# Optimization experiments

Hardware: AMD Instinct MI355X
Metric: run time of the kernel (lower is better)

Reference implementation:

```python
import jax, jax.numpy as jnp
import numpy as np

D_MODEL = 1024
N_HEAD = 16
B, T = 4, 2048


def setup_inputs() -> dict:
    key = jax.random.key(0)
    k1, k2, k3, k4, k5 = jax.random.split(key, 5)
    s = 0.02
    return {
        "x": jax.random.normal(k1, (B, T, D_MODEL), dtype=jnp.float32),
        "w_attn": jax.random.normal(k2, (3 * D_MODEL, D_MODEL), dtype=jnp.float32) * s,
        "b_attn": jax.random.normal(k3, (3 * D_MODEL,), dtype=jnp.float32) * s,
        "w_proj": jax.random.normal(k4, (D_MODEL, D_MODEL), dtype=jnp.float32) * s,
        "b_proj": jax.random.normal(k5, (D_MODEL,), dtype=jnp.float32) * s,
    }


def reference(x, w_attn, b_attn, w_proj, b_proj):
    # x: [B, T, C]
    Bb, Tt, C = x.shape
    H = N_HEAD
    dk = C // H
    scale = 1.0 / np.sqrt(dk).astype(np.float32)

    qkv = x @ w_attn.T + b_attn                      # [B, T, 3C]
    q, k, v = jnp.split(qkv, 3, axis=-1)             # each [B, T, C]
    # -> [B, H, T, dk]
    q = q.reshape(Bb, Tt, H, dk).transpose(0, 2, 1, 3)
    k = k.reshape(Bb, Tt, H, dk).transpose(0, 2, 1, 3)
    v = v.reshape(Bb, Tt, H, dk).transpose(0, 2, 1, 3)

    att = jnp.einsum("bhqd,bhkd->bhqk", q, k) * scale   # [B, H, T, T]
    att = jax.nn.softmax(att, axis=-1)
    y = jnp.einsum("bhqk,bhkd->bhqd", att, v)            # [B, H, T, dk]
    y = y.transpose(0, 2, 1, 3).reshape(Bb, Tt, C)       # [B, T, C]
    return y @ w_proj.T + b_proj
```

## Files before the change

kernel.cpp:

```cpp
#include <hip/hip_runtime.h>
#include <hip/hip_bf16.h>

typedef __attribute__((ext_vector_type(8))) short short8;
typedef __attribute__((ext_vector_type(4))) short short4v;
typedef __attribute__((ext_vector_type(4))) float floatx4;
typedef __attribute__((ext_vector_type(16))) float floatx16;

#define B_ 4
#define T_ 2048
#define C_ 1024
#define H_ 16
#define DK_ 64
#define M_ (B_ * T_)
#define N3_ (3 * C_)

#define QSCALE 0.1803368801111243f

__device__ __forceinline__ unsigned short f2bf(float f) {
    union { float f; unsigned u; } v; v.f = f;
    unsigned r = v.u + 0x7fffu + ((v.u >> 16) & 1u);
    return (unsigned short)(r >> 16);
}
__device__ __forceinline__ unsigned fbits(float f) {
    union { float f; unsigned u; } v; v.f = f; return v.u;
}
__device__ __forceinline__ unsigned pack_bf16(float a, float b) {
#if __has_builtin(__builtin_amdgcn_cvt_pk_bf16_f32)
    typedef __attribute__((ext_vector_type(2))) __bf16 bf16x2;
    bf16x2 r = __builtin_amdgcn_cvt_pk_bf16_f32(a, b);
    union { bf16x2 v; unsigned u; } c; c.v = r; return c.u;
#else
    return __builtin_amdgcn_perm(fbits(b) + 0x8000u, fbits(a) + 0x8000u, 0x07060302u);
#endif
}

__device__ __forceinline__ void gload_lds16(const unsigned short* g, unsigned short* l) {
    __builtin_amdgcn_global_load_lds(
        (const __attribute__((address_space(1))) unsigned int*)(const void*)g,
        (__attribute__((address_space(3))) unsigned int*)(void*)l, 16, 0, 0);
}

#define NX4 (M_ * C_ / 4)
#define NA4 (N3_ * C_ / 4)
#define NP4 (C_ * C_ / 4)
__global__ __launch_bounds__(256) void cast3_kernel(const float* __restrict__ x,
                                                    const float* __restrict__ wa,
                                                    const float* __restrict__ wp,
                                                    unsigned short* __restrict__ xb,
                                                    unsigned short* __restrict__ wab,
                                                    unsigned short* __restrict__ wpb) {
    int i = blockIdx.x * 256 + threadIdx.x;
    const float* src; unsigned short* dst; int j;
    if (i < NX4) { src = x; dst = xb; j = i; }
    else if (i < NX4 + NA4) { src = wa; dst = wab; j = i - NX4; }
    else { src = wp; dst = wpb; j = i - NX4 - NA4; }
    float4 v = ((const float4*)src)[j];
    ushort4 o;
    o.x = f2bf(v.x); o.y = f2bf(v.y); o.z = f2bf(v.z); o.w = f2bf(v.w);
    ((ushort4*)dst)[j] = o;
}

#define BM 128
#define BN 128
#define BK 32

__global__ __launch_bounds__(256) void gemm_qkv(const unsigned short* __restrict__ A,
                                                const unsigned short* __restrict__ W,
                                                const float* __restrict__ bias,
                                                unsigned short* __restrict__ qout,
                                                unsigned short* __restrict__ kout,
                                                unsigned short* __restrict__ vout) {
    const int Kd = C_;
    __shared__ unsigned short As[BM * BK];
    __shared__ unsigned short Bs[BN * BK];
    int m0 = blockIdx.y * BM;
    int n0 = blockIdx.x * BN;
    int tid = threadIdx.x;
    int lane = tid & 63, w = tid >> 6;
    int wm = (w >> 1) * 64, wn = (w & 1) * 64;
    int l16 = lane & 15, quad = lane >> 4;
    int r4 = lane >> 2, c4 = (lane & 3) * 8;

    floatx4 acc[4][4] = {};
    for (int kt = 0; kt < Kd; kt += BK) {
        __syncthreads();
        for (int t = 0; t < 2; ++t) {
            int rbase = w * 32 + t * 16;
            gload_lds16(&A[(size_t)(m0 + rbase + r4) * Kd + kt + c4], &As[rbase * BK]);
            gload_lds16(&W[(size_t)(n0 + rbase + r4) * Kd + kt + c4], &Bs[rbase * BK]);
        }
        __syncthreads();
        short8 af[4], bf[4];
        for (int i = 0; i < 4; ++i)
            af[i] = *(const short8*)&As[(wm + 16 * i + l16) * BK + quad * 8];
        for (int j = 0; j < 4; ++j)
            bf[j] = *(const short8*)&Bs[(wn + 16 * j + l16) * BK + quad * 8];
        for (int i = 0; i < 4; ++i)
            for (int j = 0; j < 4; ++j)
                acc[i][j] = __builtin_amdgcn_mfma_f32_16x16x32_bf16(af[i], bf[j], acc[i][j], 0, 0, 0);
    }
    for (int i = 0; i < 4; ++i)
        for (int j = 0; j < 4; ++j) {
            int col = n0 + wn + 16 * j + l16;
            float bval = bias[col];
            int sec = col >> 10, cc = col & 1023;
            int h = cc >> 6, d = cc & 63;
            float qs = (sec == 0) ? QSCALE : 1.0f;
            unsigned short* dst = (sec == 0) ? qout : ((sec == 1) ? kout : vout);
            for (int r = 0; r < 4; ++r) {
                int m = m0 + wm + 16 * i + quad * 4 + r;
                int b = m >> 11, t = m & (T_ - 1);
                int bh = b * H_ + h;
                dst[((size_t)bh * T_ + t) * DK_ + d] = f2bf((acc[i][j][r] + bval) * qs);
            }
        }
}

__global__ __launch_bounds__(256) void gemm_proj(const unsigned short* __restrict__ A,
                                                 const unsigned short* __restrict__ W,
                                                 const float* __restrict__ bias,
                                                 float* __restrict__ out) {
    const int Kd = C_;
    __shared__ unsigned short As[BM * BK];
    __shared__ unsigned short Bs[BN * BK];
    int m0 = blockIdx.y * BM;
    int n0 = blockIdx.x * BN;
    int tid = threadIdx.x;
    int lane = tid & 63, w = tid >> 6;
    int wm = (w >> 1) * 64, wn = (w & 1) * 64;
    int l16 = lane & 15, quad = lane >> 4;
    int r4 = lane >> 2, c4 = (lane & 3) * 8;

    floatx4 acc[4][4] = {};
    for (int kt = 0; kt < Kd; kt += BK) {
        __syncthreads();
        for (int t = 0; t < 2; ++t) {
            int rbase = w * 32 + t * 16;
            gload_lds16(&A[(size_t)(m0 + rbase + r4) * Kd + kt + c4], &As[rbase * BK]);
            gload_lds16(&W[(size_t)(n0 + rbase + r4) * Kd + kt + c4], &Bs[rbase * BK]);
        }
        __syncthreads();
        short8 af[4], bf[4];
        for (int i = 0; i < 4; ++i)
            af[i] = *(const short8*)&As[(wm + 16 * i + l16) * BK + quad * 8];
        for (int j = 0; j < 4; ++j)
            bf[j] = *(const short8*)&Bs[(wn + 16 * j + l16) * BK + quad * 8];
        for (int i = 0; i < 4; ++i)
            for (int j = 0; j < 4; ++j)
                acc[i][j] = __builtin_amdgcn_mfma_f32_16x16x32_bf16(af[i], bf[j], acc[i][j], 0, 0, 0);
    }
    for (int i = 0; i < 4; ++i)
        for (int j = 0; j < 4; ++j) {
            int col = n0 + wn + 16 * j + l16;
            float bval = bias[col];
            for (int r = 0; r < 4; ++r) {
                int m = m0 + wm + 16 * i + quad * 4 + r;
                out[(size_t)m * C_ + col] = acc[i][j][r] + bval;
            }
        }
}

#define TLD 258
__global__ __launch_bounds__(256) void vtrans_kernel(const unsigned short* __restrict__ V,
                                                     unsigned short* __restrict__ Vt) {
    __shared__ unsigned short L[64 * TLD];
    int bid = blockIdx.x;
    int t0 = (bid & 7) * 256;
    int bh = bid >> 3;
    int tid = threadIdx.x;
    const unsigned short* src = V + ((size_t)bh * T_ + t0) * DK_;
    unsigned short* dst = Vt + (size_t)bh * DK_ * T_ + t0;
    for (int it = 0; it < 8; ++it) {
        int t = it * 32 + (tid >> 3);
        int dseg = (tid & 7) * 8;
        short8 v = *(const short8*)&src[(size_t)t * DK_ + dseg];
        for (int j = 0; j < 8; ++j)
            L[(dseg + j) * TLD + t] = ((unsigned short*)&v)[j];
    }
    __syncthreads();
    for (int it = 0; it < 8; ++it) {
        int d = it * 8 + (tid >> 5);
        int toff = (tid & 31) * 8;
        short8 r = *(const short8*)&L[d * TLD + toff];
        *(short8*)&dst[(size_t)d * T_ + toff] = r;
    }
}

#define KT 64
#define LD 72

__global__ __launch_bounds__(256, 2) void attn_kernel(const unsigned short* __restrict__ Q,
                                                      const unsigned short* __restrict__ Kv,
                                                      const unsigned short* __restrict__ Vt,
                                                      unsigned short* __restrict__ Y) {
    __shared__ unsigned short smem[128 * LD];
    unsigned short* Ks = smem;
    unsigned short* Vts = smem + 64 * LD;

    int bid = blockIdx.x;
    int qt = bid & 7;
    int bh = bid >> 3;
    int b = bh >> 4, hh = bh & 15;
    const unsigned short* qh = Q + (size_t)bh * T_ * DK_;
    const unsigned short* kh = Kv + (size_t)bh * T_ * DK_;
    const unsigned short* vtg = Vt + (size_t)bh * DK_ * T_;

    int tid = threadIdx.x, lane = tid & 63, w = tid >> 6;
    int l31 = lane & 31, h = lane >> 5;
    int qrA = qt * 256 + w * 32;
    int qrB = qrA + 128;

    short8 qfA[4], qfB[4];
    for (int c = 0; c < 4; ++c) {
        qfA[c] = *(const short8*)&qh[(size_t)(qrA + l31) * DK_ + 16 * c + 8 * h];
        qfB[c] = *(const short8*)&qh[(size_t)(qrB + l31) * DK_ + 16 * c + 8 * h];
    }

    floatx16 oA0 = {}, oA1 = {}, oB0 = {}, oB1 = {};
    float lA = 0.f, lB = 0.f;

    for (int kt = 0; kt < T_; kt += KT) {
        __syncthreads();
        for (int it = 0; it < 2; ++it) {
            int idx = tid + it * 256;
            int r8 = idx >> 3, c8 = (idx & 7) * 8;
            *(short8*)&Ks[r8 * LD + c8] = *(const short8*)&kh[(size_t)(kt + r8) * DK_ + c8];
            *(short8*)&Vts[r8 * LD + c8] = *(const short8*)&vtg[(size_t)r8 * T_ + kt + c8];
        }
        __syncthreads();

        floatx16 sA0 = {}, sA1 = {}, sB0 = {}, sB1 = {};
        for (int c = 0; c < 4; ++c) {
            short8 kf0 = *(const short8*)&Ks[l31 * LD + 16 * c + 8 * h];
            short8 kf1 = *(const short8*)&Ks[(32 + l31) * LD + 16 * c + 8 * h];
            sA0 = __builtin_amdgcn_mfma_f32_32x32x16_bf16(kf0, qfA[c], sA0, 0, 0, 0);
            sA1 = __builtin_amdgcn_mfma_f32_32x32x16_bf16(kf1, qfA[c], sA1, 0, 0, 0);
            sB0 = __builtin_amdgcn_mfma_f32_32x32x16_bf16(kf0, qfB[c], sB0, 0, 0, 0);
            sB1 = __builtin_amdgcn_mfma_f32_32x32x16_bf16(kf1, qfB[c], sB1, 0, 0, 0);
        }

        unsigned pA[16], pB[16];
        float tsA = 0.f, tsB = 0.f;
        for (int r2 = 0; r2 < 8; ++r2) {
            float a0 = __builtin_amdgcn_exp2f(sA0[2 * r2]);
            float a1 = __builtin_amdgcn_exp2f(sA0[2 * r2 + 1]);
            tsA += a0 + a1; pA[r2] = pack_bf16(a0, a1);
            float a2 = __builtin_amdgcn_exp2f(sA1[2 * r2]);
            float a3 = __builtin_amdgcn_exp2f(sA1[2 * r2 + 1]);
            tsA += a2 + a3; pA[8 + r2] = pack_bf16(a2, a3);
            float b0 = __builtin_amdgcn_exp2f(sB0[2 * r2]);
            float b1 = __builtin_amdgcn_exp2f(sB0[2 * r2 + 1]);
            tsB += b0 + b1; pB[r2] = pack_bf16(b0, b1);
            float b2 = __builtin_amdgcn_exp2f(sB1[2 * r2]);
            float b3 = __builtin_amdgcn_exp2f(sB1[2 * r2 + 1]);
            tsB += b2 + b3; pB[8 + r2] = pack_bf16(b2, b3);
        }
        lA += tsA; lB += tsB;

        for (int c = 0; c < 4; ++c) {
            short8 vf0, vf1;
            {
                short4v lo0 = *(const short4v*)&Vts[l31 * LD + 16 * c + 4 * h];
                short4v hi0 = *(const short4v*)&Vts[l31 * LD + 16 * c + 8 + 4 * h];
                short4v lo1 = *(const short4v*)&Vts[(32 + l31) * LD + 16 * c + 4 * h];
                short4v hi1 = *(const short4v*)&Vts[(32 + l31) * LD + 16 * c + 8 + 4 * h];
                for (int j = 0; j < 4; ++j) {
                    vf0[j] = lo0[j]; vf0[4 + j] = hi0[j];
                    vf1[j] = lo1[j]; vf1[4 + j] = hi1[j];
                }
            }
            union { unsigned u[4]; short8 s; } fA, fB;
            for (int j = 0; j < 4; ++j) { fA.u[j] = pA[4 * c + j]; fB.u[j] = pB[4 * c + j]; }
            oA0 = __builtin_amdgcn_mfma_f32_32x32x16_bf16(vf0, fA.s, oA0, 0, 0, 0);
            oA1 = __builtin_amdgcn_mfma_f32_32x32x16_bf16(vf1, fA.s, oA1, 0, 0, 0);
            oB0 = __builtin_amdgcn_mfma_f32_32x32x16_bf16(vf0, fB.s, oB0, 0, 0, 0);
            oB1 = __builtin_amdgcn_mfma_f32_32x32x16_bf16(vf1, fB.s, oB1, 0, 0, 0);
        }
    }

    float invA = 1.0f / (lA + __shfl_xor(lA, 32, 64));
    float invB = 1.0f / (lB + __shfl_xor(lB, 32, 64));
    int q_l = tid >> 1, seg = tid & 1;

    __syncthreads();
    for (int a = 0; a < 4; ++a) {
        ushort4 u;
        u.x = f2bf(oA0[4 * a + 0] * invA); u.y = f2bf(oA0[4 * a + 1] * invA);
        u.z = f2bf(oA0[4 * a + 2] * invA); u.w = f2bf(oA0[4 * a + 3] * invA);
        *(ushort4*)&smem[(w * 32 + l31) * LD + 8 * a + 4 * h] = u;
        ushort4 v;
        v.x = f2bf(oA1[4 * a + 0] * invA); v.y = f2bf(oA1[4 * a + 1] * invA);
        v.z = f2bf(oA1[4 * a + 2] * invA); v.w = f2bf(oA1[4 * a + 3] * invA);
        *(ushort4*)&smem[(w * 32 + l31) * LD + 32 + 8 * a + 4 * h] = v;
    }
    __syncthreads();
    {
        const unsigned short* srcp = &smem[(size_t)q_l * LD + seg * 32];
        unsigned short* dstp = &Y[((size_t)b * T_ + qt * 256 + q_l) * C_ + hh * DK_ + seg * 32];
        for (int j = 0; j < 4; ++j)
            *(short8*)&dstp[8 * j] = *(const short8*)&srcp[8 * j];
    }
    __syncthreads();
    for (int a = 0; a < 4; ++a) {
        ushort4 u;
        u.x = f2bf(oB0[4 * a + 0] * invB); u.y = f2bf(oB0[4 * a + 1] * invB);
        u.z = f2bf(oB0[4 * a + 2] * invB); u.w = f2bf(oB0[4 * a + 3] * invB);
        *(ushort4*)&smem[(w * 32 + l31) * LD + 8 * a + 4 * h] = u;
        ushort4 v;
        v.x = f2bf(oB1[4 * a + 0] * invB); v.y = f2bf(oB1[4 * a + 1] * invB);
        v.z = f2bf(oB1[4 * a + 2] * invB); v.w = f2bf(oB1[4 * a + 3] * invB);
        *(ushort4*)&smem[(w * 32 + l31) * LD + 32 + 8 * a + 4 * h] = v;
    }
    __syncthreads();
    {
        const unsigned short* srcp = &smem[(size_t)q_l * LD + seg * 32];
        unsigned short* dstp = &Y[((size_t)b * T_ + qt * 256 + 128 + q_l) * C_ + hh * DK_ + seg * 32];
        for (int j = 0; j < 4; ++j)
            *(short8*)&dstp[8 * j] = *(const short8*)&srcp[8 * j];
    }
}

extern "C" void kernel_launch(void* const* d_in, const int* in_sizes, int n_in,
                              void* d_out, int out_size, void* d_ws, size_t ws_size,
                              hipStream_t stream) {
    const float* x      = (const float*)d_in[0];
    const float* w_attn = (const float*)d_in[1];
    const float* b_attn = (const float*)d_in[2];
    const float* w_proj = (const float*)d_in[3];
    const float* b_proj = (const float*)d_in[4];
    float* out = (float*)d_out;

    unsigned short* ws = (unsigned short*)d_ws;
    unsigned short* xb  = ws;
    unsigned short* wab = xb  + (size_t)M_ * C_;
    unsigned short* wpb = wab + (size_t)N3_ * C_;
    unsigned short* qb  = wpb + (size_t)C_ * C_;
    unsigned short* kb  = qb  + (size_t)M_ * C_;
    unsigned short* vb  = kb  + (size_t)M_ * C_;
    unsigned short* yb  = vb  + (size_t)M_ * C_;
    unsigned short* vtb = xb;

    cast3_kernel<<<(NX4 + NA4 + NP4) / 256, 256, 0, stream>>>(x, w_attn, w_proj, xb, wab, wpb);
    gemm_qkv<<<dim3(N3_ / BN, M_ / BM), 256, 0, stream>>>(xb, wab, b_attn, qb, kb, vb);
    vtrans_kernel<<<B_ * H_ * (T_ / 256), 256, 0, stream>>>(vb, vtb);
    attn_kernel<<<B_ * H_ * (T_ / 256), 256, 0, stream>>>(qb, kb, vtb, yb);
    gemm_proj<<<dim3(C_ / BN, M_ / BM), 256, 0, stream>>>(yb, wpb, b_proj, out);
}
```

Measured before the change: 272.7 us.

## Double-buffer K/V tiles with register prefetch and compute row sums via MFMA

```diff
diff --git a/kernel.cpp b/kernel.cpp
--- a/kernel.cpp
+++ b/kernel.cpp
@@ -188,14 +188,13 @@
 
 #define KT 64
 #define LD 72
+#define BUFH (128 * LD)
 
 __global__ __launch_bounds__(256, 2) void attn_kernel(const unsigned short* __restrict__ Q,
                                                       const unsigned short* __restrict__ Kv,
                                                       const unsigned short* __restrict__ Vt,
                                                       unsigned short* __restrict__ Y) {
-    __shared__ unsigned short smem[128 * LD];
-    unsigned short* Ks = smem;
-    unsigned short* Vts = smem + 64 * LD;
+    __shared__ unsigned short smem[2 * BUFH];
 
     int bid = blockIdx.x;
     int qt = bid & 7;
@@ -210,26 +209,55 @@
     int qrA = qt * 256 + w * 32;
     int qrB = qrA + 128;
 
+    int r80 = tid >> 3, c80 = (tid & 7) * 8;
+    int r81 = (tid + 256) >> 3, c81 = ((tid + 256) & 7) * 8;
+    int vd0 = r80 * LD + (c80 & 48) + ((c80 & 8) >> 1);
+    int vd1 = r81 * LD + (c81 & 48) + ((c81 & 8) >> 1);
+
     short8 qfA[4], qfB[4];
     for (int c = 0; c < 4; ++c) {
         qfA[c] = *(const short8*)&qh[(size_t)(qrA + l31) * DK_ + 16 * c + 8 * h];
         qfB[c] = *(const short8*)&qh[(size_t)(qrB + l31) * DK_ + 16 * c + 8 * h];
     }
 
+    short8 ones;
+    for (int j = 0; j < 8; ++j) ones[j] = (short)0x3F80;
+
     floatx16 oA0 = {}, oA1 = {}, oB0 = {}, oB1 = {};
-    float lA = 0.f, lB = 0.f;
-
+    floatx16 oLA = {}, oLB = {};
+
+    {
+        short8 k0 = *(const short8*)&kh[(size_t)r80 * DK_ + c80];
+        short8 k1 = *(const short8*)&kh[(size_t)r81 * DK_ + c81];
+        short8 v0 = *(const short8*)&vtg[(size_t)r80 * T_ + c80];
+        short8 v1 = *(const short8*)&vtg[(size_t)r81 * T_ + c81];
+        unsigned short* Ks = smem;
+        unsigned short* Vts = smem + 64 * LD;
+        *(short8*)&Ks[r80 * LD + c80] = k0;
+        *(short8*)&Ks[r81 * LD + c81] = k1;
+        union { short8 s; short4v q[2]; } u0, u1;
+        u0.s = v0; u1.s = v1;
+        *(short4v*)&Vts[vd0] = u0.q[0]; *(short4v*)&Vts[vd0 + 8] = u0.q[1];
+        *(short4v*)&Vts[vd1] = u1.q[0]; *(short4v*)&Vts[vd1 + 8] = u1.q[1];
+    }
+
+    int cur = 0;
     for (int kt = 0; kt < T_; kt += KT) {
         __syncthreads();
-        for (int it = 0; it < 2; ++it) {
-            int idx = tid + it * 256;
-            int r8 = idx >> 3, c8 = (idx & 7) * 8;
-            *(short8*)&Ks[r8 * LD + c8] = *(const short8*)&kh[(size_t)(kt + r8) * DK_ + c8];
-            *(short8*)&Vts[r8 * LD + c8] = *(const short8*)&vtg[(size_t)r8 * T_ + kt + c8];
-        }
-        __syncthreads();
+        const unsigned short* Ks = smem + cur * BUFH;
+        const unsigned short* Vts = Ks + 64 * LD;
+
+        bool pre = (kt + KT < T_);
+        short8 nk0, nk1, nv0, nv1;
+        if (pre) {
+            nk0 = *(const short8*)&kh[(size_t)(kt + KT + r80) * DK_ + c80];
+            nk1 = *(const short8*)&kh[(size_t)(kt + KT + r81) * DK_ + c81];
+            nv0 = *(const short8*)&vtg[(size_t)r80 * T_ + kt + KT + c80];
+            nv1 = *(const short8*)&vtg[(size_t)r81 * T_ + kt + KT + c81];
+        }
 
         floatx16 sA0 = {}, sA1 = {}, sB0 = {}, sB1 = {};
+        __builtin_amdgcn_s_setprio(1);
         for (int c = 0; c < 4; ++c) {
             short8 kf0 = *(const short8*)&Ks[l31 * LD + 16 * c + 8 * h];
             short8 kf1 = *(const short8*)&Ks[(32 + l31) * LD + 16 * c + 8 * h];
@@ -238,48 +266,50 @@
             sB0 = __builtin_amdgcn_mfma_f32_32x32x16_bf16(kf0, qfB[c], sB0, 0, 0, 0);
             sB1 = __builtin_amdgcn_mfma_f32_32x32x16_bf16(kf1, qfB[c], sB1, 0, 0, 0);
         }
+        __builtin_amdgcn_s_setprio(0);
 
         unsigned pA[16], pB[16];
-        float tsA = 0.f, tsB = 0.f;
         for (int r2 = 0; r2 < 8; ++r2) {
-            float a0 = __builtin_amdgcn_exp2f(sA0[2 * r2]);
-            float a1 = __builtin_amdgcn_exp2f(sA0[2 * r2 + 1]);
-            tsA += a0 + a1; pA[r2] = pack_bf16(a0, a1);
-            float a2 = __builtin_amdgcn_exp2f(sA1[2 * r2]);
-            float a3 = __builtin_amdgcn_exp2f(sA1[2 * r2 + 1]);
-            tsA += a2 + a3; pA[8 + r2] = pack_bf16(a2, a3);
-            float b0 = __builtin_amdgcn_exp2f(sB0[2 * r2]);
-            float b1 = __builtin_amdgcn_exp2f(sB0[2 * r2 + 1]);
-            tsB += b0 + b1; pB[r2] = pack_bf16(b0, b1);
-            float b2 = __builtin_amdgcn_exp2f(sB1[2 * r2]);
-            float b3 = __builtin_amdgcn_exp2f(sB1[2 * r2 + 1]);
-            tsB += b2 + b3; pB[8 + r2] = pack_bf16(b2, b3);
-        }
-        lA += tsA; lB += tsB;
-
+            pA[r2]     = pack_bf16(__builtin_amdgcn_exp2f(sA0[2 * r2]),
+                                   __builtin_amdgcn_exp2f(sA0[2 * r2 + 1]));
+            pA[8 + r2] = pack_bf16(__builtin_amdgcn_exp2f(sA1[2 * r2]),
+                                   __builtin_amdgcn_exp2f(sA1[2 * r2 + 1]));
+            pB[r2]     = pack_bf16(__builtin_amdgcn_exp2f(sB0[2 * r2]),
+                                   __builtin_amdgcn_exp2f(sB0[2 * r2 + 1]));
+            pB[8 + r2] = pack_bf16(__builtin_amdgcn_exp2f(sB1[2 * r2]),
+                                   __builtin_amdgcn_exp2f(sB1[2 * r2 + 1]));
+        }
+
+        __builtin_amdgcn_s_setprio(1);
         for (int c = 0; c < 4; ++c) {
-            short8 vf0, vf1;
-            {
-                short4v lo0 = *(const short4v*)&Vts[l31 * LD + 16 * c + 4 * h];
-                short4v hi0 = *(const short4v*)&Vts[l31 * LD + 16 * c + 8 + 4 * h];
-                short4v lo1 = *(const short4v*)&Vts[(32 + l31) * LD + 16 * c + 4 * h];
-                short4v hi1 = *(const short4v*)&Vts[(32 + l31) * LD + 16 * c + 8 + 4 * h];
-                for (int j = 0; j < 4; ++j) {
-                    vf0[j] = lo0[j]; vf0[4 + j] = hi0[j];
-                    vf1[j] = lo1[j]; vf1[4 + j] = hi1[j];
-                }
-            }
+            short8 vf0 = *(const short8*)&Vts[l31 * LD + 16 * c + 8 * h];
+            short8 vf1 = *(const short8*)&Vts[(32 + l31) * LD + 16 * c + 8 * h];
             union { unsigned u[4]; short8 s; } fA, fB;
             for (int j = 0; j < 4; ++j) { fA.u[j] = pA[4 * c + j]; fB.u[j] = pB[4 * c + j]; }
             oA0 = __builtin_amdgcn_mfma_f32_32x32x16_bf16(vf0, fA.s, oA0, 0, 0, 0);
             oA1 = __builtin_amdgcn_mfma_f32_32x32x16_bf16(vf1, fA.s, oA1, 0, 0, 0);
             oB0 = __builtin_amdgcn_mfma_f32_32x32x16_bf16(vf0, fB.s, oB0, 0, 0, 0);
             oB1 = __builtin_amdgcn_mfma_f32_32x32x16_bf16(vf1, fB.s, oB1, 0, 0, 0);
-        }
-    }
-
-    float invA = 1.0f / (lA + __shfl_xor(lA, 32, 64));
-    float invB = 1.0f / (lB + __shfl_xor(lB, 32, 64));
+            oLA = __builtin_amdgcn_mfma_f32_32x32x16_bf16(ones, fA.s, oLA, 0, 0, 0);
+            oLB = __builtin_amdgcn_mfma_f32_32x32x16_bf16(ones, fB.s, oLB, 0, 0, 0);
+        }
+        __builtin_amdgcn_s_setprio(0);
+
+        if (pre) {
+            unsigned short* Ksn = smem + (cur ^ 1) * BUFH;
+            unsigned short* Vtsn = Ksn + 64 * LD;
+            *(short8*)&Ksn[r80 * LD + c80] = nk0;
+            *(short8*)&Ksn[r81 * LD + c81] = nk1;
+            union { short8 s; short4v q[2]; } u0, u1;
+            u0.s = nv0; u1.s = nv1;
+            *(short4v*)&Vtsn[vd0] = u0.q[0]; *(short4v*)&Vtsn[vd0 + 8] = u0.q[1];
+            *(short4v*)&Vtsn[vd1] = u1.q[0]; *(short4v*)&Vtsn[vd1 + 8] = u1.q[1];
+        }
+        cur ^= 1;
+    }
+
+    float invA = 1.0f / oLA[0];
+    float invB = 1.0f / oLB[0];
     int q_l = tid >> 1, seg = tid & 1;
 
     __syncthreads();
```

Result: no change. 270.4 us (-0.8%).

## Swizzle GEMM block order across XCDs and pre-permute V tile in LDS

Applied to the files above, without the earlier changes.

```diff
diff --git a/kernel.cpp b/kernel.cpp
--- a/kernel.cpp
+++ b/kernel.cpp
@@ -73,8 +73,11 @@
     const int Kd = C_;
     __shared__ unsigned short As[BM * BK];
     __shared__ unsigned short Bs[BN * BK];
-    int m0 = blockIdx.y * BM;
-    int n0 = blockIdx.x * BN;
+    int lin = blockIdx.y * gridDim.x + blockIdx.x;
+    int cpx = (gridDim.x * gridDim.y) >> 3;
+    int swz = (lin & 7) * cpx + (lin >> 3);
+    int m0 = (swz / gridDim.x) * BM;
+    int n0 = (swz % gridDim.x) * BN;
     int tid = threadIdx.x;
     int lane = tid & 63, w = tid >> 6;
     int wm = (w >> 1) * 64, wn = (w & 1) * 64;
@@ -123,8 +126,11 @@
     const int Kd = C_;
     __shared__ unsigned short As[BM * BK];
     __shared__ unsigned short Bs[BN * BK];
-    int m0 = blockIdx.y * BM;
-    int n0 = blockIdx.x * BN;
+    int lin = blockIdx.y * gridDim.x + blockIdx.x;
+    int cpx = (gridDim.x * gridDim.y) >> 3;
+    int swz = (lin & 7) * cpx + (lin >> 3);
+    int m0 = (swz / gridDim.x) * BM;
+    int n0 = (swz % gridDim.x) * BN;
     int tid = threadIdx.x;
     int lane = tid & 63, w = tid >> 6;
     int wm = (w >> 1) * 64, wn = (w & 1) * 64;
@@ -225,7 +231,11 @@
             int idx = tid + it * 256;
             int r8 = idx >> 3, c8 = (idx & 7) * 8;
             *(short8*)&Ks[r8 * LD + c8] = *(const short8*)&kh[(size_t)(kt + r8) * DK_ + c8];
-            *(short8*)&Vts[r8 * LD + c8] = *(const short8*)&vtg[(size_t)r8 * T_ + kt + c8];
+            int vd = r8 * LD + (c8 & 48) + ((c8 & 8) >> 1);
+            union { short8 s; short4v q[2]; } u;
+            u.s = *(const short8*)&vtg[(size_t)r8 * T_ + kt + c8];
+            *(short4v*)&Vts[vd] = u.q[0];
+            *(short4v*)&Vts[vd + 8] = u.q[1];
         }
         __syncthreads();
 
@@ -258,17 +268,8 @@
         lA += tsA; lB += tsB;
 
         for (int c = 0; c < 4; ++c) {
-            short8 vf0, vf1;
-            {
-                short4v lo0 = *(const short4v*)&Vts[l31 * LD + 16 * c + 4 * h];
-                short4v hi0 = *(const short4v*)&Vts[l31 * LD + 16 * c + 8 + 4 * h];
-                short4v lo1 = *(const short4v*)&Vts[(32 + l31) * LD + 16 * c + 4 * h];
-                short4v hi1 = *(const short4v*)&Vts[(32 + l31) * LD + 16 * c + 8 + 4 * h];
-                for (int j = 0; j < 4; ++j) {
-                    vf0[j] = lo0[j]; vf0[4 + j] = hi0[j];
-                    vf1[j] = lo1[j]; vf1[4 + j] = hi1[j];
-                }
-            }
+            short8 vf0 = *(const short8*)&Vts[l31 * LD + 16 * c + 8 * h];
+            short8 vf1 = *(const short8*)&Vts[(32 + l31) * LD + 16 * c + 8 * h];
             union { unsigned u[4]; short8 s; } fA, fB;
             for (int j = 0; j < 4; ++j) { fA.u[j] = pA[4 * c + j]; fB.u[j] = pB[4 * c + j]; }
             oA0 = __builtin_amdgcn_mfma_f32_32x32x16_bf16(vf0, fA.s, oA0, 0, 0, 0);
```

Result: no change. 272.4 us (-0.1%).
